# Optimization experiments

Measured on AMD Instinct MI355X. Metric: run time of the kernel, lower is better.

Reference implementation:

```python
import jax, jax.numpy as jnp
import numpy as np

EMB_DIM = 768
HEADS = 12
HEAD_DIM = EMB_DIM // HEADS  # 64


def setup_inputs() -> dict:
    key = jax.random.key(0)
    ks = jax.random.split(key, 9)
    s = 1.0 / np.sqrt(EMB_DIM)
    d = dict(
        x=jax.random.normal(ks[0], (2, 2048, EMB_DIM), dtype=jnp.float32),
        wq_w=jax.random.normal(ks[1], (EMB_DIM, EMB_DIM), dtype=jnp.float32) * s,
        wq_b=jax.random.normal(ks[2], (EMB_DIM,), dtype=jnp.float32) * 0.01,
        wk_w=jax.random.normal(ks[3], (EMB_DIM, EMB_DIM), dtype=jnp.float32) * s,
        wk_b=jax.random.normal(ks[4], (EMB_DIM,), dtype=jnp.float32) * 0.01,
        wv_w=jax.random.normal(ks[5], (EMB_DIM, EMB_DIM), dtype=jnp.float32) * s,
        wv_b=jax.random.normal(ks[6], (EMB_DIM,), dtype=jnp.float32) * 0.01,
        wo_w=jax.random.normal(ks[7], (EMB_DIM, EMB_DIM), dtype=jnp.float32) * s,
        wo_b=jax.random.normal(ks[8], (EMB_DIM,), dtype=jnp.float32) * 0.01,
    )
    return d


def reference(x, wq_w, wq_b, wk_w, wk_b, wv_w, wv_b, wo_w, wo_b):
    b, n, _ = x.shape
    # Linear projections (torch Linear: x @ W^T + b). q scaled by 1/8 == 1/sqrt(head_dim).
    q = (x @ wq_w.T + wq_b) / 8.0
    k = x @ wk_w.T + wk_b
    v = x @ wv_w.T + wv_b
    # [b, h, n, d]
    q = q.reshape(b, n, HEADS, HEAD_DIM).transpose(0, 2, 1, 3)
    k = k.reshape(b, n, HEADS, HEAD_DIM).transpose(0, 2, 1, 3)
    v = v.reshape(b, n, HEADS, HEAD_DIM).transpose(0, 2, 1, 3)
    # Full [b, h, n, n] score matrix with causal mask (strict upper triangle = -inf)
    scores = jnp.einsum('bhqd,bhkd->bhqk', q, k)
    causal = jnp.tril(jnp.ones((n, n), dtype=bool))  # True where allowed
    scores = jnp.where(causal[None, None], scores, -jnp.inf)
    attn = jax.nn.softmax(scores, axis=-1)
    out = jnp.einsum('bhqk,bhkd->bhqd', attn, v)
    out = out.transpose(0, 2, 1, 3).reshape(b, n, EMB_DIM)
    return out @ wo_w.T + wo_b
```

## Files before the change

kernel.cpp:

```cpp
#include <hip/hip_runtime.h>
#include <hip/hip_bf16.h>
#include <math.h>

#define EMB  768
#define NH   12
#define HD   64
#define SEQ  2048
#define BATCH 2
#define NTOK 4096

typedef __attribute__((ext_vector_type(8))) short short8;
typedef __attribute__((ext_vector_type(4))) float float4v;

static __device__ __forceinline__ short f2bf(float f) {
    __hip_bfloat16 h = __float2bfloat16(f);
    return *reinterpret_cast<short*>(&h);
}

static __device__ __forceinline__ void gll16(const void* g, void* l) {
    __builtin_amdgcn_global_load_lds(
        (const __attribute__((address_space(1))) void*)g,
        (__attribute__((address_space(3))) void*)l, 16, 0, 0);
}

__global__ __launch_bounds__(256) void cast_kernel(
    const float* __restrict__ x,  const float* __restrict__ wq,
    const float* __restrict__ wk, const float* __restrict__ wv,
    const float* __restrict__ wo,
    __hip_bfloat16* __restrict__ xb,  __hip_bfloat16* __restrict__ wqb,
    __hip_bfloat16* __restrict__ wkb, __hip_bfloat16* __restrict__ wvb,
    __hip_bfloat16* __restrict__ wob)
{
    const size_t S0 = (size_t)NTOK * EMB;
    const size_t S1 = (size_t)EMB * EMB;
    size_t i = ((size_t)blockIdx.x * 256 + threadIdx.x) * 8;
    const float* src; __hip_bfloat16* dst; size_t off;
    if      (i < S0)            { src = x;  dst = xb;  off = i; }
    else if (i < S0 + S1)       { src = wq; dst = wqb; off = i - S0; }
    else if (i < S0 + 2 * S1)   { src = wk; dst = wkb; off = i - S0 - S1; }
    else if (i < S0 + 3 * S1)   { src = wv; dst = wvb; off = i - S0 - 2 * S1; }
    else                        { src = wo; dst = wob; off = i - S0 - 3 * S1; }
    float4 f0 = *(const float4*)&src[off];
    float4 f1 = *(const float4*)&src[off + 4];
    short8 o;
    o[0] = f2bf(f0.x); o[1] = f2bf(f0.y); o[2] = f2bf(f0.z); o[3] = f2bf(f0.w);
    o[4] = f2bf(f1.x); o[5] = f2bf(f1.y); o[6] = f2bf(f1.z); o[7] = f2bf(f1.w);
    *(short8*)&dst[off] = o;
}

__global__ __launch_bounds__(256) void qkv_mfma_kernel(
    const __hip_bfloat16* __restrict__ xb,
    const __hip_bfloat16* __restrict__ wqb, const float* __restrict__ bq,
    const __hip_bfloat16* __restrict__ wkb, const float* __restrict__ bk,
    const __hip_bfloat16* __restrict__ wvb, const float* __restrict__ bv,
    __hip_bfloat16* __restrict__ q, __hip_bfloat16* __restrict__ k,
    __hip_bfloat16* __restrict__ vT)
{
    __shared__ __align__(16) short SM[12288];
    short* As = SM;
    short* Bs = SM + 4096;
    const int t = threadIdx.x;
    const int w = t >> 6, lane = t & 63;
    const int col = lane & 15, quad = lane >> 4;
    const int wm = w >> 1, wn = w & 1;
    const int m0 = blockIdx.y * 64;
    const int mat = blockIdx.x / 6;
    const int jj0 = (blockIdx.x % 6) * 128;
    const short* X = (const short*)xb;
    const short* W = (const short*)((mat == 0) ? wqb : (mat == 1) ? wkb : wvb);
    const float* bias = (mat == 0) ? bq : (mat == 1) ? bk : bv;

    float4v acc[2][4];
    #pragma unroll
    for (int mi = 0; mi < 2; ++mi)
        #pragma unroll
        for (int ni = 0; ni < 4; ++ni) acc[mi][ni] = (float4v){0.f, 0.f, 0.f, 0.f};

    for (int kb = 0; kb < EMB; kb += 64) {
        #pragma unroll
        for (int c = 0; c < 2; ++c) {
            int I = w * 128 + c * 64 + lane;
            int row = I >> 3;
            int c8 = (I & 7) ^ (row & 7);
            gll16(X + (size_t)(m0 + row) * EMB + kb + c8 * 8,
                  &As[(w * 128 + c * 64) * 8]);
        }
        #pragma unroll
        for (int c = 0; c < 4; ++c) {
            int I = w * 256 + c * 64 + lane;
            int row = I >> 3;
            int c8 = (I & 7) ^ (row & 7);
            gll16(W + (size_t)(jj0 + row) * EMB + kb + c8 * 8,
                  &Bs[(w * 256 + c * 64) * 8]);
        }
        __syncthreads();
        #pragma unroll
        for (int ks = 0; ks < 2; ++ks) {
            short8 a[2], b[4];
            #pragma unroll
            for (int mi = 0; mi < 2; ++mi) {
                int row = wm * 32 + mi * 16 + col;
                a[mi] = *(short8*)&As[row * 64 + (((ks * 4 + quad) ^ (row & 7)) * 8)];
            }
            #pragma unroll
            for (int ni = 0; ni < 4; ++ni) {
                int row = wn * 64 + ni * 16 + col;
                b[ni] = *(short8*)&Bs[row * 64 + (((ks * 4 + quad) ^ (row & 7)) * 8)];
            }
            #pragma unroll
            for (int mi = 0; mi < 2; ++mi)
                #pragma unroll
                for (int ni = 0; ni < 4; ++ni)
                    acc[mi][ni] = __builtin_amdgcn_mfma_f32_16x16x32_bf16(
                        a[mi], b[ni], acc[mi][ni], 0, 0, 0);
        }
        __syncthreads();
    }
    const int bi = m0 >> 11, n0g = m0 & (SEQ - 1);
    if (mat != 2) {
        const float scale = (mat == 0) ? 0.125f * 1.44269504088896f : 1.0f;
        __hip_bfloat16* dstqk = (mat == 0) ? q : k;
        #pragma unroll
        for (int mi = 0; mi < 2; ++mi)
            #pragma unroll
            for (int ni = 0; ni < 4; ++ni) {
                int gj_l = wn * 64 + ni * 16 + col;
                float bsv = bias[jj0 + gj_l];
                #pragma unroll
                for (int r = 0; r < 4; ++r) {
                    int n_l = wm * 32 + mi * 16 + quad * 4 + r;
                    int cswz = (gj_l >> 3) ^ (n_l & 15);
                    SM[(n_l << 7) + (cswz << 3) + (gj_l & 7)] =
                        f2bf((acc[mi][ni][r] + bsv) * scale);
                }
            }
        __syncthreads();
        #pragma unroll
        for (int it = 0; it < 4; ++it) {
            int I = it * 256 + t;
            int n_l = I >> 4, c = I & 15;
            short8 val = *(short8*)&SM[(n_l << 7) + ((c ^ (n_l & 15)) << 3)];
            int gj = jj0 + c * 8;
            int h = gj >> 6, d0 = gj & 63;
            int gm = m0 + n_l;
            int bb = gm >> 11, n = gm & (SEQ - 1);
            *(short8*)&dstqk[(((size_t)bb * NH + h) * SEQ + n) * HD + d0] = val;
        }
    } else {
        #pragma unroll
        for (int mi = 0; mi < 2; ++mi)
            #pragma unroll
            for (int ni = 0; ni < 4; ++ni) {
                int d_l = wn * 64 + ni * 16 + col;
                float bsv = bias[jj0 + d_l];
                #pragma unroll
                for (int r = 0; r < 4; ++r) {
                    int n_l = wm * 32 + mi * 16 + quad * 4 + r;
                    int cn = n_l >> 3;
                    SM[(d_l << 6) + (((cn ^ (d_l & 7))) << 3) + (n_l & 7)] =
                        f2bf(acc[mi][ni][r] + bsv);
                }
            }
        __syncthreads();
        #pragma unroll
        for (int it = 0; it < 4; ++it) {
            int I = it * 256 + t;
            int d_l = I >> 3, cn = I & 7;
            short8 val = *(short8*)&SM[(d_l << 6) + ((cn ^ (d_l & 7)) << 3)];
            int gj = jj0 + d_l;
            int h = gj >> 6, dd = gj & 63;
            *(short8*)&vT[(((size_t)bi * NH + h) * HD + dd) * SEQ + n0g + cn * 8] = val;
        }
    }
}

__global__ __launch_bounds__(256) void attn_mfma_kernel(
    const __hip_bfloat16* __restrict__ qg, const __hip_bfloat16* __restrict__ kg,
    const __hip_bfloat16* __restrict__ vTg, __hip_bfloat16* __restrict__ ao,
    float* __restrict__ Os0, float* __restrict__ Os1,
    float* __restrict__ l0, float* __restrict__ l1)
{
    __shared__ __align__(16) short Ks[2][64 * 64];
    __shared__ __align__(16) short Vt[2][64 * 64];
    __shared__ __align__(16) short Ps[4][32][72];
    const int t = threadIdx.x;
    const int w = t >> 6, lane = t & 63;
    const int col = lane & 15, quad = lane >> 4;
    const int id = blockIdx.x;
    const int bh = id % 24;
    const int x = id / 24;
    int b, c;
    if (x < 8) { b = 8 + x; c = 0; }
    else {
        int i = x - 8, j = i >> 1;
        if ((i & 1) == 0) { b = 7 - j;  c = 0; }
        else              { b = 15 - j; c = 1; }
    }
    const int kt0 = c * 16;
    const int ktend = (kt0 + 16 < 2 * b + 2) ? kt0 + 16 : 2 * b + 2;
    const int niter = ktend - kt0;
    const bool single = (b <= 7);
    const int q0 = b * 128;
    const size_t base = (size_t)bh * SEQ * HD;
    const short* kp = (const short*)kg + base;
    const short* vp = (const short*)vTg + base;
    const short* qp = (const short*)qg + base;

    short8 qa[2][2];
    #pragma unroll
    for (int mi = 0; mi < 2; ++mi) {
        int qrow = q0 + (2 * w + mi) * 16 + col;
        #pragma unroll
        for (int ks = 0; ks < 2; ++ks)
            qa[mi][ks] = *(const short8*)&qp[(size_t)qrow * HD + ks * 32 + quad * 8];
    }
    float4v accO[2][4];
    float lacc[2][4];
    #pragma unroll
    for (int mi = 0; mi < 2; ++mi) {
        #pragma unroll
        for (int di = 0; di < 4; ++di) accO[mi][di] = (float4v){0.f, 0.f, 0.f, 0.f};
        #pragma unroll
        for (int r = 0; r < 4; ++r) lacc[mi][r] = 0.f;
    }

    {
        const int k0 = kt0 * 64;
        #pragma unroll
        for (int cc = 0; cc < 2; ++cc) {
            int I = w * 128 + cc * 64 + lane;
            int row = I >> 3;
            int c8 = (I & 7) ^ (row & 7);
            gll16(kp + (size_t)(k0 + row) * HD + c8 * 8, &Ks[0][(w * 128 + cc * 64) * 8]);
            gll16(vp + (size_t)row * SEQ + k0 + c8 * 8, &Vt[0][(w * 128 + cc * 64) * 8]);
        }
    }

    for (int lk = 0; lk < niter; ++lk) {
        const int kt = kt0 + lk;
        const int cur = lk & 1;
        const int k0 = kt * 64;
        __syncthreads();
        if (lk + 1 < niter) {
            const int kn = k0 + 64;
            #pragma unroll
            for (int cc = 0; cc < 2; ++cc) {
                int I = w * 128 + cc * 64 + lane;
                int row = I >> 3;
                int c8 = (I & 7) ^ (row & 7);
                gll16(kp + (size_t)(kn + row) * HD + c8 * 8,
                      &Ks[cur ^ 1][(w * 128 + cc * 64) * 8]);
                gll16(vp + (size_t)row * SEQ + kn + c8 * 8,
                      &Vt[cur ^ 1][(w * 128 + cc * 64) * 8]);
            }
        }
        const short* Kc = &Ks[cur][0];
        const short* Vc = &Vt[cur][0];

        float4v s[2][4];
        #pragma unroll
        for (int mi = 0; mi < 2; ++mi)
            #pragma unroll
            for (int ni = 0; ni < 4; ++ni) s[mi][ni] = (float4v){0.f, 0.f, 0.f, 0.f};
        #pragma unroll
        for (int ks = 0; ks < 2; ++ks)
            #pragma unroll
            for (int ni = 0; ni < 4; ++ni) {
                int row = ni * 16 + col;
                short8 kf = *(short8*)&Kc[row * 64 + (((ks * 4 + quad) ^ (row & 7)) * 8)];
                #pragma unroll
                for (int mi = 0; mi < 2; ++mi)
                    s[mi][ni] = __builtin_amdgcn_mfma_f32_16x16x32_bf16(
                        qa[mi][ks], kf, s[mi][ni], 0, 0, 0);
            }

        if (k0 >= q0) {
            #pragma unroll
            for (int mi = 0; mi < 2; ++mi)
                #pragma unroll
                for (int ni = 0; ni < 4; ++ni) {
                    int gcol = k0 + ni * 16 + col;
                    #pragma unroll
                    for (int r = 0; r < 4; ++r) {
                        int grow = q0 + (2 * w + mi) * 16 + quad * 4 + r;
                        s[mi][ni][r] = (gcol > grow) ? 0.f : exp2f(s[mi][ni][r]);
                    }
                }
        } else {
            #pragma unroll
            for (int mi = 0; mi < 2; ++mi)
                #pragma unroll
                for (int ni = 0; ni < 4; ++ni)
                    #pragma unroll
                    for (int r = 0; r < 4; ++r)
                        s[mi][ni][r] = exp2f(s[mi][ni][r]);
        }
        #pragma unroll
        for (int mi = 0; mi < 2; ++mi)
            #pragma unroll
            for (int r = 0; r < 4; ++r)
                lacc[mi][r] += (s[mi][0][r] + s[mi][1][r]) + (s[mi][2][r] + s[mi][3][r]);

        #pragma unroll
        for (int mi = 0; mi < 2; ++mi)
            #pragma unroll
            for (int ni = 0; ni < 4; ++ni)
                #pragma unroll
                for (int r = 0; r < 4; ++r)
                    Ps[w][mi * 16 + quad * 4 + r][ni * 16 + col] = f2bf(s[mi][ni][r]);
        short8 pa[2][2];
        #pragma unroll
        for (int mi = 0; mi < 2; ++mi)
            #pragma unroll
            for (int ks = 0; ks < 2; ++ks)
                pa[mi][ks] = *(short8*)&Ps[w][mi * 16 + col][ks * 32 + quad * 8];

        #pragma unroll
        for (int ks = 0; ks < 2; ++ks)
            #pragma unroll
            for (int di = 0; di < 4; ++di) {
                int row = di * 16 + col;
                short8 vf = *(short8*)&Vc[row * 64 + (((ks * 4 + quad) ^ (row & 7)) * 8)];
                #pragma unroll
                for (int mi = 0; mi < 2; ++mi)
                    accO[mi][di] = __builtin_amdgcn_mfma_f32_16x16x32_bf16(
                        pa[mi][ks], vf, accO[mi][di], 0, 0, 0);
            }
    }

    #pragma unroll
    for (int msk = 1; msk < 16; msk <<= 1)
        #pragma unroll
        for (int mi = 0; mi < 2; ++mi)
            #pragma unroll
            for (int r = 0; r < 4; ++r)
                lacc[mi][r] += __shfl_xor(lacc[mi][r], msk);

    const int bi = bh / NH, h = bh % NH;
    if (single) {
        #pragma unroll
        for (int mi = 0; mi < 2; ++mi)
            #pragma unroll
            for (int r = 0; r < 4; ++r) {
                float inv = 1.0f / lacc[mi][r];
                int n = q0 + (2 * w + mi) * 16 + quad * 4 + r;
                #pragma unroll
                for (int di = 0; di < 4; ++di)
                    ao[((size_t)bi * SEQ + n) * EMB + h * HD + di * 16 + col] =
                        __float2bfloat16(accO[mi][di][r] * inv);
            }
    } else {
        float* Os = c ? Os1 : Os0;
        float* ls = c ? l1 : l0;
        #pragma unroll
        for (int mi = 0; mi < 2; ++mi)
            #pragma unroll
            for (int r = 0; r < 4; ++r) {
                int n = q0 + (2 * w + mi) * 16 + quad * 4 + r;
                int nn = n - 1024;
                size_t rowb = ((size_t)bi * 1024 + nn) * EMB + h * HD;
                #pragma unroll
                for (int di = 0; di < 4; ++di)
                    Os[rowb + di * 16 + col] = accO[mi][di][r];
                if (col == 0)
                    ls[((size_t)bi * 1024 + nn) * NH + h] = lacc[mi][r];
            }
    }
}

__global__ __launch_bounds__(256) void combine_kernel(
    const float* __restrict__ Os0, const float* __restrict__ Os1,
    const float* __restrict__ l0, const float* __restrict__ l1,
    __hip_bfloat16* __restrict__ ao)
{
    size_t e8 = ((size_t)blockIdx.x * 256 + threadIdx.x) * 8;
    int u = e8 / EMB;
    int within = e8 % EMB;
    int h = within >> 6;
    int bi = u >> 10, nn = u & 1023;
    float inv = 1.0f / (l0[(size_t)u * NH + h] + l1[(size_t)u * NH + h]);
    float4 a0 = *(const float4*)&Os0[e8];
    float4 a1 = *(const float4*)&Os0[e8 + 4];
    float4 b0 = *(const float4*)&Os1[e8];
    float4 b1 = *(const float4*)&Os1[e8 + 4];
    short8 o;
    o[0] = f2bf((a0.x + b0.x) * inv); o[1] = f2bf((a0.y + b0.y) * inv);
    o[2] = f2bf((a0.z + b0.z) * inv); o[3] = f2bf((a0.w + b0.w) * inv);
    o[4] = f2bf((a1.x + b1.x) * inv); o[5] = f2bf((a1.y + b1.y) * inv);
    o[6] = f2bf((a1.z + b1.z) * inv); o[7] = f2bf((a1.w + b1.w) * inv);
    *(short8*)&ao[((size_t)bi * SEQ + 1024 + nn) * EMB + within] = o;
}

__global__ __launch_bounds__(256) void out_proj_mfma_kernel(
    const __hip_bfloat16* __restrict__ a, const __hip_bfloat16* __restrict__ wob,
    const float* __restrict__ bias, float* __restrict__ out)
{
    __shared__ __align__(16) short As[64 * 64];
    __shared__ __align__(16) short Bs[64 * 64];
    const int t = threadIdx.x;
    const int w = t >> 6, lane = t & 63;
    const int col = lane & 15, quad = lane >> 4;
    const int wm = w >> 1, wn = w & 1;
    const int m0 = blockIdx.y * 64;
    const int n0 = blockIdx.x * 64;
    const short* A = (const short*)a;
    const short* W = (const short*)wob;

    float4v acc[2][2];
    #pragma unroll
    for (int mi = 0; mi < 2; ++mi)
        #pragma unroll
        for (int ni = 0; ni < 2; ++ni) acc[mi][ni] = (float4v){0.f, 0.f, 0.f, 0.f};

    for (int kb = 0; kb < EMB; kb += 64) {
        #pragma unroll
        for (int c = 0; c < 2; ++c) {
            int I = w * 128 + c * 64 + lane;
            int row = I >> 3;
            int c8 = (I & 7) ^ (row & 7);
            gll16(A + (size_t)(m0 + row) * EMB + kb + c8 * 8,
                  &As[(w * 128 + c * 64) * 8]);
            gll16(W + (size_t)(n0 + row) * EMB + kb + c8 * 8,
                  &Bs[(w * 128 + c * 64) * 8]);
        }
        __syncthreads();
        #pragma unroll
        for (int ks = 0; ks < 2; ++ks) {
            short8 av[2], bv[2];
            #pragma unroll
            for (int mi = 0; mi < 2; ++mi) {
                int row = wm * 32 + mi * 16 + col;
                av[mi] = *(short8*)&As[row * 64 + (((ks * 4 + quad) ^ (row & 7)) * 8)];
            }
            #pragma unroll
            for (int ni = 0; ni < 2; ++ni) {
                int row = wn * 32 + ni * 16 + col;
                bv[ni] = *(short8*)&Bs[row * 64 + (((ks * 4 + quad) ^ (row & 7)) * 8)];
            }
            #pragma unroll
            for (int mi = 0; mi < 2; ++mi)
                #pragma unroll
                for (int ni = 0; ni < 2; ++ni)
                    acc[mi][ni] = __builtin_amdgcn_mfma_f32_16x16x32_bf16(
                        av[mi], bv[ni], acc[mi][ni], 0, 0, 0);
        }
        __syncthreads();
    }
    #pragma unroll
    for (int mi = 0; mi < 2; ++mi)
        #pragma unroll
        for (int ni = 0; ni < 2; ++ni) {
            int gj = n0 + wn * 32 + ni * 16 + col;
            float bsv = bias[gj];
            #pragma unroll
            for (int r = 0; r < 4; ++r) {
                int gm = m0 + wm * 32 + mi * 16 + quad * 4 + r;
                out[(size_t)gm * EMB + gj] = acc[mi][ni][r] + bsv;
            }
        }
}

extern "C" void kernel_launch(void* const* d_in, const int* in_sizes, int n_in,
                              void* d_out, int out_size, void* d_ws, size_t ws_size,
                              hipStream_t stream) {
    const float* x  = (const float*)d_in[0];
    const float* wq = (const float*)d_in[1];
    const float* bq = (const float*)d_in[2];
    const float* wk = (const float*)d_in[3];
    const float* bk = (const float*)d_in[4];
    const float* wv = (const float*)d_in[5];
    const float* bv = (const float*)d_in[6];
    const float* wo = (const float*)d_in[7];
    const float* bo = (const float*)d_in[8];
    float* out = (float*)d_out;

    const size_t TOK = (size_t)NTOK * EMB;
    const size_t WSZ = (size_t)EMB * EMB;
    __hip_bfloat16* xb  = (__hip_bfloat16*)d_ws;
    __hip_bfloat16* wqb = xb  + TOK;
    __hip_bfloat16* wkb = wqb + WSZ;
    __hip_bfloat16* wvb = wkb + WSZ;
    __hip_bfloat16* wob = wvb + WSZ;
    __hip_bfloat16* qb  = wob + WSZ;
    __hip_bfloat16* kb  = qb  + TOK;
    __hip_bfloat16* vTb = kb  + TOK;
    __hip_bfloat16* aob = vTb + TOK;
    float* Os0 = (float*)d_ws;
    float* Os1 = (float*)(aob + TOK);
    float* l0  = Os1 + (size_t)2 * 1024 * EMB;
    float* l1  = l0  + (size_t)2 * 1024 * NH;

    cast_kernel<<<2688, 256, 0, stream>>>(x, wq, wk, wv, wo, xb, wqb, wkb, wvb, wob);
    qkv_mfma_kernel<<<dim3(18, 64), 256, 0, stream>>>(xb, wqb, bq, wkb, bk, wvb, bv,
                                                      qb, kb, vTb);
    attn_mfma_kernel<<<576, 256, 0, stream>>>(qb, kb, vTb, aob, Os0, Os1, l0, l1);
    combine_kernel<<<768, 256, 0, stream>>>(Os0, Os1, l0, l1, aob);
    out_proj_mfma_kernel<<<dim3(12, 64), 256, 0, stream>>>(aob, wob, bo, out);
}
```

Before: 164.7 us.

## Use 256-row query blocks with up to four key-chunk splits in attention

Attention blocks now cover 256 query rows (64 per wave) instead of 128, and the key range is split into chunks of 8 tiles, giving up to four partial results per block that the combine kernel sums. This doubles Q reuse per loaded K/V tile and interleaves the QK and PV matmuls per 32-key half with a smaller P scratch buffer. Waves skip tiles lying fully above their diagonal. In exchange it writes and reads more fp32 partials in workspace, uses more registers per thread, and launches fewer attention blocks.

Measured after the change: 186.9 us. +13.5%, slower.

```diff
diff --git a/kernel.cpp b/kernel.cpp
--- a/kernel.cpp
+++ b/kernel.cpp
@@ -22,6 +22,9 @@
         (const __attribute__((address_space(1))) void*)g,
         (__attribute__((address_space(3))) void*)l, 16, 0, 0);
 }
+
+__device__ const int BS8[16] = {1,2,3,3,4,4,5,5,5,6,6,6,7,7,7,7};
+__device__ const int CS8[16] = {0,0,0,1,0,1,0,1,2,0,1,2,0,1,2,3};
 
 __global__ __launch_bounds__(256) void cast_kernel(
     const float* __restrict__ x,  const float* __restrict__ wq,
@@ -177,12 +180,11 @@
 __global__ __launch_bounds__(256) void attn_mfma_kernel(
     const __hip_bfloat16* __restrict__ qg, const __hip_bfloat16* __restrict__ kg,
     const __hip_bfloat16* __restrict__ vTg, __hip_bfloat16* __restrict__ ao,
-    float* __restrict__ Os0, float* __restrict__ Os1,
-    float* __restrict__ l0, float* __restrict__ l1)
+    float* __restrict__ Osp, float* __restrict__ lsp)
 {
-    __shared__ __align__(16) short Ks[2][64 * 64];
-    __shared__ __align__(16) short Vt[2][64 * 64];
-    __shared__ __align__(16) short Ps[4][32][72];
+    __shared__ __align__(16) short Ks[2][4096];
+    __shared__ __align__(16) short Vt[2][4096];
+    __shared__ __align__(16) short Ps[4][64 * 40];
     const int t = threadIdx.x;
     const int w = t >> 6, lane = t & 63;
     const int col = lane & 15, quad = lane >> 4;
@@ -190,34 +192,31 @@
     const int bh = id % 24;
     const int x = id / 24;
     int b, c;
-    if (x < 8) { b = 8 + x; c = 0; }
-    else {
-        int i = x - 8, j = i >> 1;
-        if ((i & 1) == 0) { b = 7 - j;  c = 0; }
-        else              { b = 15 - j; c = 1; }
-    }
-    const int kt0 = c * 16;
-    const int ktend = (kt0 + 16 < 2 * b + 2) ? kt0 + 16 : 2 * b + 2;
-    const int niter = ktend - kt0;
-    const bool single = (b <= 7);
-    const int q0 = b * 128;
+    if (x < 16) { b = BS8[x]; c = CS8[x]; }
+    else        { int i = x - 16; b = 2 * i; c = i; }
+    const int kt0 = c * 8;
+    const int tottiles = 4 * b + 4;
+    const int niter = (tottiles - kt0 < 8) ? (tottiles - kt0) : 8;
+    const bool single = (b <= 1);
+    const int q0 = b * 256;
     const size_t base = (size_t)bh * SEQ * HD;
     const short* kp = (const short*)kg + base;
     const short* vp = (const short*)vTg + base;
     const short* qp = (const short*)qg + base;
-
-    short8 qa[2][2];
-    #pragma unroll
-    for (int mi = 0; mi < 2; ++mi) {
-        int qrow = q0 + (2 * w + mi) * 16 + col;
+    const int rw = q0 + w * 64;
+
+    short8 qa[4][2];
+    #pragma unroll
+    for (int mi = 0; mi < 4; ++mi) {
+        int qrow = rw + mi * 16 + col;
         #pragma unroll
         for (int ks = 0; ks < 2; ++ks)
             qa[mi][ks] = *(const short8*)&qp[(size_t)qrow * HD + ks * 32 + quad * 8];
     }
-    float4v accO[2][4];
-    float lacc[2][4];
-    #pragma unroll
-    for (int mi = 0; mi < 2; ++mi) {
+    float4v accO[4][4];
+    float lacc[4][4];
+    #pragma unroll
+    for (int mi = 0; mi < 4; ++mi) {
         #pragma unroll
         for (int di = 0; di < 4; ++di) accO[mi][di] = (float4v){0.f, 0.f, 0.f, 0.f};
         #pragma unroll
@@ -254,84 +253,70 @@
                       &Vt[cur ^ 1][(w * 128 + cc * 64) * 8]);
             }
         }
+        if (k0 > rw) continue;
+        const bool diag = (k0 == rw);
         const short* Kc = &Ks[cur][0];
         const short* Vc = &Vt[cur][0];
-
-        float4v s[2][4];
-        #pragma unroll
-        for (int mi = 0; mi < 2; ++mi)
-            #pragma unroll
-            for (int ni = 0; ni < 4; ++ni) s[mi][ni] = (float4v){0.f, 0.f, 0.f, 0.f};
-        #pragma unroll
-        for (int ks = 0; ks < 2; ++ks)
-            #pragma unroll
-            for (int ni = 0; ni < 4; ++ni) {
-                int row = ni * 16 + col;
-                short8 kf = *(short8*)&Kc[row * 64 + (((ks * 4 + quad) ^ (row & 7)) * 8)];
-                #pragma unroll
-                for (int mi = 0; mi < 2; ++mi)
-                    s[mi][ni] = __builtin_amdgcn_mfma_f32_16x16x32_bf16(
-                        qa[mi][ks], kf, s[mi][ni], 0, 0, 0);
-            }
-
-        if (k0 >= q0) {
-            #pragma unroll
-            for (int mi = 0; mi < 2; ++mi)
-                #pragma unroll
-                for (int ni = 0; ni < 4; ++ni) {
-                    int gcol = k0 + ni * 16 + col;
+        short* Pw = &Ps[w][0];
+
+        #pragma unroll
+        for (int ni = 0; ni < 4; ++ni) {
+            float4v s[4];
+            #pragma unroll
+            for (int mi = 0; mi < 4; ++mi) s[mi] = (float4v){0.f, 0.f, 0.f, 0.f};
+            int krow = ni * 16 + col;
+            #pragma unroll
+            for (int ks = 0; ks < 2; ++ks) {
+                short8 kf = *(short8*)&Kc[krow * 64 + (((ks * 4 + quad) ^ (krow & 7)) * 8)];
+                #pragma unroll
+                for (int mi = 0; mi < 4; ++mi)
+                    s[mi] = __builtin_amdgcn_mfma_f32_16x16x32_bf16(
+                        qa[mi][ks], kf, s[mi], 0, 0, 0);
+            }
+            if (diag) {
+                int gcol = k0 + ni * 16 + col;
+                #pragma unroll
+                for (int mi = 0; mi < 4; ++mi)
                     #pragma unroll
                     for (int r = 0; r < 4; ++r) {
-                        int grow = q0 + (2 * w + mi) * 16 + quad * 4 + r;
-                        s[mi][ni][r] = (gcol > grow) ? 0.f : exp2f(s[mi][ni][r]);
+                        int grow = rw + mi * 16 + quad * 4 + r;
+                        float p = (gcol > grow) ? 0.f : exp2f(s[mi][r]);
+                        lacc[mi][r] += p;
+                        Pw[(mi * 16 + quad * 4 + r) * 40 + (ni & 1) * 16 + col] = f2bf(p);
                     }
+            } else {
+                #pragma unroll
+                for (int mi = 0; mi < 4; ++mi)
+                    #pragma unroll
+                    for (int r = 0; r < 4; ++r) {
+                        float p = exp2f(s[mi][r]);
+                        lacc[mi][r] += p;
+                        Pw[(mi * 16 + quad * 4 + r) * 40 + (ni & 1) * 16 + col] = f2bf(p);
+                    }
+            }
+            if (ni & 1) {
+                const int half = ni >> 1;
+                short8 pa[4];
+                #pragma unroll
+                for (int mi = 0; mi < 4; ++mi)
+                    pa[mi] = *(short8*)&Pw[(mi * 16 + col) * 40 + quad * 8];
+                #pragma unroll
+                for (int di = 0; di < 4; ++di) {
+                    int vrow = di * 16 + col;
+                    short8 vf = *(short8*)&Vc[vrow * 64 + (((half * 4 + quad) ^ (vrow & 7)) * 8)];
+                    #pragma unroll
+                    for (int mi = 0; mi < 4; ++mi)
+                        accO[mi][di] = __builtin_amdgcn_mfma_f32_16x16x32_bf16(
+                            pa[mi], vf, accO[mi][di], 0, 0, 0);
                 }
-        } else {
-            #pragma unroll
-            for (int mi = 0; mi < 2; ++mi)
-                #pragma unroll
-                for (int ni = 0; ni < 4; ++ni)
-                    #pragma unroll
-                    for (int r = 0; r < 4; ++r)
-                        s[mi][ni][r] = exp2f(s[mi][ni][r]);
-        }
-        #pragma unroll
-        for (int mi = 0; mi < 2; ++mi)
-            #pragma unroll
-            for (int r = 0; r < 4; ++r)
-                lacc[mi][r] += (s[mi][0][r] + s[mi][1][r]) + (s[mi][2][r] + s[mi][3][r]);
-
-        #pragma unroll
-        for (int mi = 0; mi < 2; ++mi)
-            #pragma unroll
-            for (int ni = 0; ni < 4; ++ni)
-                #pragma unroll
-                for (int r = 0; r < 4; ++r)
-                    Ps[w][mi * 16 + quad * 4 + r][ni * 16 + col] = f2bf(s[mi][ni][r]);
-        short8 pa[2][2];
-        #pragma unroll
-        for (int mi = 0; mi < 2; ++mi)
-            #pragma unroll
-            for (int ks = 0; ks < 2; ++ks)
-                pa[mi][ks] = *(short8*)&Ps[w][mi * 16 + col][ks * 32 + quad * 8];
-
-        #pragma unroll
-        for (int ks = 0; ks < 2; ++ks)
-            #pragma unroll
-            for (int di = 0; di < 4; ++di) {
-                int row = di * 16 + col;
-                short8 vf = *(short8*)&Vc[row * 64 + (((ks * 4 + quad) ^ (row & 7)) * 8)];
-                #pragma unroll
-                for (int mi = 0; mi < 2; ++mi)
-                    accO[mi][di] = __builtin_amdgcn_mfma_f32_16x16x32_bf16(
-                        pa[mi][ks], vf, accO[mi][di], 0, 0, 0);
-            }
+            }
+        }
     }
 
     #pragma unroll
     for (int msk = 1; msk < 16; msk <<= 1)
         #pragma unroll
-        for (int mi = 0; mi < 2; ++mi)
+        for (int mi = 0; mi < 4; ++mi)
             #pragma unroll
             for (int r = 0; r < 4; ++r)
                 lacc[mi][r] += __shfl_xor(lacc[mi][r], msk);
@@ -339,56 +324,67 @@
     const int bi = bh / NH, h = bh % NH;
     if (single) {
         #pragma unroll
-        for (int mi = 0; mi < 2; ++mi)
+        for (int mi = 0; mi < 4; ++mi)
             #pragma unroll
             for (int r = 0; r < 4; ++r) {
                 float inv = 1.0f / lacc[mi][r];
-                int n = q0 + (2 * w + mi) * 16 + quad * 4 + r;
+                int n = rw + mi * 16 + quad * 4 + r;
                 #pragma unroll
                 for (int di = 0; di < 4; ++di)
                     ao[((size_t)bi * SEQ + n) * EMB + h * HD + di * 16 + col] =
                         __float2bfloat16(accO[mi][di][r] * inv);
             }
     } else {
-        float* Os = c ? Os1 : Os0;
-        float* ls = c ? l1 : l0;
-        #pragma unroll
-        for (int mi = 0; mi < 2; ++mi)
+        float* Os = Osp + (size_t)c * 2 * 1536 * EMB;
+        float* ls = lsp + (size_t)c * 2 * 1536 * NH;
+        #pragma unroll
+        for (int mi = 0; mi < 4; ++mi)
             #pragma unroll
             for (int r = 0; r < 4; ++r) {
-                int n = q0 + (2 * w + mi) * 16 + quad * 4 + r;
-                int nn = n - 1024;
-                size_t rowb = ((size_t)bi * 1024 + nn) * EMB + h * HD;
+                int n = rw + mi * 16 + quad * 4 + r;
+                int nn = n - 512;
+                size_t rowb = ((size_t)bi * 1536 + nn) * EMB + h * HD;
                 #pragma unroll
                 for (int di = 0; di < 4; ++di)
                     Os[rowb + di * 16 + col] = accO[mi][di][r];
                 if (col == 0)
-                    ls[((size_t)bi * 1024 + nn) * NH + h] = lacc[mi][r];
+                    ls[((size_t)bi * 1536 + nn) * NH + h] = lacc[mi][r];
             }
     }
 }
 
 __global__ __launch_bounds__(256) void combine_kernel(
-    const float* __restrict__ Os0, const float* __restrict__ Os1,
-    const float* __restrict__ l0, const float* __restrict__ l1,
+    const float* __restrict__ Osp, const float* __restrict__ lsp,
     __hip_bfloat16* __restrict__ ao)
 {
+    const size_t SLOT = (size_t)2 * 1536 * EMB;
+    const size_t LSLOT = (size_t)2 * 1536 * NH;
     size_t e8 = ((size_t)blockIdx.x * 256 + threadIdx.x) * 8;
     int u = e8 / EMB;
     int within = e8 % EMB;
     int h = within >> 6;
-    int bi = u >> 10, nn = u & 1023;
-    float inv = 1.0f / (l0[(size_t)u * NH + h] + l1[(size_t)u * NH + h]);
-    float4 a0 = *(const float4*)&Os0[e8];
-    float4 a1 = *(const float4*)&Os0[e8 + 4];
-    float4 b0 = *(const float4*)&Os1[e8];
-    float4 b1 = *(const float4*)&Os1[e8 + 4];
+    int bi = u / 1536, nn = u % 1536;
+    int n = 512 + nn;
+    int qb = n >> 8;
+    int nc = (qb >> 1) + 1;
+    float4 a0 = *(const float4*)&Osp[e8];
+    float4 a1 = *(const float4*)&Osp[e8 + 4];
+    float lsum = lsp[(size_t)u * NH + h];
+    for (int cc = 1; cc < nc; ++cc) {
+        const float* O = Osp + (size_t)cc * SLOT;
+        float4 b0 = *(const float4*)&O[e8];
+        float4 b1 = *(const float4*)&O[e8 + 4];
+        a0.x += b0.x; a0.y += b0.y; a0.z += b0.z; a0.w += b0.w;
+        a1.x += b1.x; a1.y += b1.y; a1.z += b1.z; a1.w += b1.w;
+        lsum += lsp[(size_t)cc * LSLOT + (size_t)u * NH + h];
+    }
+    float inv = 1.0f / lsum;
     short8 o;
-    o[0] = f2bf((a0.x + b0.x) * inv); o[1] = f2bf((a0.y + b0.y) * inv);
-    o[2] = f2bf((a0.z + b0.z) * inv); o[3] = f2bf((a0.w + b0.w) * inv);
-    o[4] = f2bf((a1.x + b1.x) * inv); o[5] = f2bf((a1.y + b1.y) * inv);
-    o[6] = f2bf((a1.z + b1.z) * inv); o[7] = f2bf((a1.w + b1.w) * inv);
-    *(short8*)&ao[((size_t)bi * SEQ + 1024 + nn) * EMB + within] = o;
+    o[0] = f2bf(a0.x * inv); o[1] = f2bf(a0.y * inv);
+    o[2] = f2bf(a0.z * inv); o[3] = f2bf(a0.w * inv);
+    o[4] = f2bf(a1.x * inv); o[5] = f2bf(a1.y * inv);
+    o[6] = f2bf(a1.z * inv); o[7] = f2bf(a1.w * inv);
+    *(short8*)&ao[((size_t)bi * SEQ + n) * EMB + within] = o;
 }
 
 __global__ __launch_bounds__(256) void out_proj_mfma_kernel(
@@ -485,15 +481,13 @@
     __hip_bfloat16* kb  = qb  + TOK;
     __hip_bfloat16* vTb = kb  + TOK;
     __hip_bfloat16* aob = vTb + TOK;
-    float* Os0 = (float*)d_ws;
-    float* Os1 = (float*)(aob + TOK);
-    float* l0  = Os1 + (size_t)2 * 1024 * EMB;
-    float* l1  = l0  + (size_t)2 * 1024 * NH;
+    float* Osp = (float*)(aob + TOK);
+    float* lsp = Osp + (size_t)4 * 2 * 1536 * EMB;
 
     cast_kernel<<<2688, 256, 0, stream>>>(x, wq, wk, wv, wo, xb, wqb, wkb, wvb, wob);
     qkv_mfma_kernel<<<dim3(18, 64), 256, 0, stream>>>(xb, wqb, bq, wkb, bk, wvb, bv,
                                                       qb, kb, vTb);
-    attn_mfma_kernel<<<576, 256, 0, stream>>>(qb, kb, vTb, aob, Os0, Os1, l0, l1);
-    combine_kernel<<<768, 256, 0, stream>>>(Os0, Os1, l0, l1, aob);
+    attn_mfma_kernel<<<480, 256, 0, stream>>>(qb, kb, vTb, aob, Osp, lsp);
+    combine_kernel<<<1152, 256, 0, stream>>>(Osp, lsp, aob);
     out_proj_mfma_kernel<<<dim3(12, 64), 256, 0, stream>>>(aob, wob, bo, out);
 }
```

## Split causal attention KV range into four chunks with table-driven scheduling

Applied to the files above, without the earlier changes.

Changes the split-K attention from two KV halves of 16 tiles to up to four chunks of 8 tiles each. Query blocks 4 and above are split, and a lookup table orders the work items so the longest ones are scheduled first. The goal is to even out per-block work and raise the block count (576 to 960) for better CU utilization on the causal triangle. In exchange, more fp32 partial results must be written and then reduced by a larger combine kernel, which adds memory traffic and workspace.

After: 160.6 us. -2.5%, faster.

```diff
diff --git a/kernel.cpp b/kernel.cpp
--- a/kernel.cpp
+++ b/kernel.cpp
@@ -22,6 +22,23 @@
         (const __attribute__((address_space(1))) void*)g,
         (__attribute__((address_space(3))) void*)l, 16, 0, 0);
 }
+
+__device__ const unsigned char UB[40] = {
+    3,4,5,6,7,8,9,10,11,12,13,14,15,
+    7,8,9,10,11,12,13,14,15,
+    11,12,13,14,15,
+    15,
+    2,6,10,14,
+    1,5,9,13,
+    0,4,8,12};
+__device__ const unsigned char UC[40] = {
+    0,0,0,0,0,0,0,0,0,0,0,0,0,
+    1,1,1,1,1,1,1,1,1,
+    2,2,2,2,2,
+    3,
+    0,1,2,3,
+    0,1,2,3,
+    0,1,2,3};
 
 __global__ __launch_bounds__(256) void cast_kernel(
     const float* __restrict__ x,  const float* __restrict__ wq,
@@ -177,8 +194,7 @@
 __global__ __launch_bounds__(256) void attn_mfma_kernel(
     const __hip_bfloat16* __restrict__ qg, const __hip_bfloat16* __restrict__ kg,
     const __hip_bfloat16* __restrict__ vTg, __hip_bfloat16* __restrict__ ao,
-    float* __restrict__ Os0, float* __restrict__ Os1,
-    float* __restrict__ l0, float* __restrict__ l1)
+    float* __restrict__ Osp, float* __restrict__ lsp)
 {
     __shared__ __align__(16) short Ks[2][64 * 64];
     __shared__ __align__(16) short Vt[2][64 * 64];
@@ -189,17 +205,11 @@
     const int id = blockIdx.x;
     const int bh = id % 24;
     const int x = id / 24;
-    int b, c;
-    if (x < 8) { b = 8 + x; c = 0; }
-    else {
-        int i = x - 8, j = i >> 1;
-        if ((i & 1) == 0) { b = 7 - j;  c = 0; }
-        else              { b = 15 - j; c = 1; }
-    }
-    const int kt0 = c * 16;
-    const int ktend = (kt0 + 16 < 2 * b + 2) ? kt0 + 16 : 2 * b + 2;
-    const int niter = ktend - kt0;
-    const bool single = (b <= 7);
+    const int b = UB[x], c = UC[x];
+    const int kt0 = c * 8;
+    const int tottiles = 2 * b + 2;
+    const int niter = (tottiles - kt0 < 8) ? (tottiles - kt0) : 8;
+    const bool single = (b <= 3);
     const int q0 = b * 128;
     const size_t base = (size_t)bh * SEQ * HD;
     const short* kp = (const short*)kg + base;
@@ -350,45 +360,56 @@
                         __float2bfloat16(accO[mi][di][r] * inv);
             }
     } else {
-        float* Os = c ? Os1 : Os0;
-        float* ls = c ? l1 : l0;
+        float* Os = Osp + (size_t)c * 2 * 1536 * EMB;
+        float* ls = lsp + (size_t)c * 2 * 1536 * NH;
         #pragma unroll
         for (int mi = 0; mi < 2; ++mi)
             #pragma unroll
             for (int r = 0; r < 4; ++r) {
                 int n = q0 + (2 * w + mi) * 16 + quad * 4 + r;
-                int nn = n - 1024;
-                size_t rowb = ((size_t)bi * 1024 + nn) * EMB + h * HD;
+                int nn = n - 512;
+                size_t rowb = ((size_t)bi * 1536 + nn) * EMB + h * HD;
                 #pragma unroll
                 for (int di = 0; di < 4; ++di)
                     Os[rowb + di * 16 + col] = accO[mi][di][r];
                 if (col == 0)
-                    ls[((size_t)bi * 1024 + nn) * NH + h] = lacc[mi][r];
+                    ls[((size_t)bi * 1536 + nn) * NH + h] = lacc[mi][r];
             }
     }
 }
 
 __global__ __launch_bounds__(256) void combine_kernel(
-    const float* __restrict__ Os0, const float* __restrict__ Os1,
-    const float* __restrict__ l0, const float* __restrict__ l1,
+    const float* __restrict__ Osp, const float* __restrict__ lsp,
     __hip_bfloat16* __restrict__ ao)
 {
+    const size_t SLOT = (size_t)2 * 1536 * EMB;
+    const size_t LSLOT = (size_t)2 * 1536 * NH;
     size_t e8 = ((size_t)blockIdx.x * 256 + threadIdx.x) * 8;
     int u = e8 / EMB;
     int within = e8 % EMB;
     int h = within >> 6;
-    int bi = u >> 10, nn = u & 1023;
-    float inv = 1.0f / (l0[(size_t)u * NH + h] + l1[(size_t)u * NH + h]);
-    float4 a0 = *(const float4*)&Os0[e8];
-    float4 a1 = *(const float4*)&Os0[e8 + 4];
-    float4 b0 = *(const float4*)&Os1[e8];
-    float4 b1 = *(const float4*)&Os1[e8 + 4];
+    int bi = u / 1536, nn = u % 1536;
+    int n = 512 + nn;
+    int qb = n >> 7;
+    int nc = (2 * qb + 9) >> 3;
+    float4 a0 = *(const float4*)&Osp[e8];
+    float4 a1 = *(const float4*)&Osp[e8 + 4];
+    float lsum = lsp[(size_t)u * NH + h];
+    for (int cc = 1; cc < nc; ++cc) {
+        const float* O = Osp + (size_t)cc * SLOT;
+        float4 b0 = *(const float4*)&O[e8];
+        float4 b1 = *(const float4*)&O[e8 + 4];
+        a0.x += b0.x; a0.y += b0.y; a0.z += b0.z; a0.w += b0.w;
+        a1.x += b1.x; a1.y += b1.y; a1.z += b1.z; a1.w += b1.w;
+        lsum += lsp[(size_t)cc * LSLOT + (size_t)u * NH + h];
+    }
+    float inv = 1.0f / lsum;
     short8 o;
-    o[0] = f2bf((a0.x + b0.x) * inv); o[1] = f2bf((a0.y + b0.y) * inv);
-    o[2] = f2bf((a0.z + b0.z) * inv); o[3] = f2bf((a0.w + b0.w) * inv);
-    o[4] = f2bf((a1.x + b1.x) * inv); o[5] = f2bf((a1.y + b1.y) * inv);
-    o[6] = f2bf((a1.z + b1.z) * inv); o[7] = f2bf((a1.w + b1.w) * inv);
-    *(short8*)&ao[((size_t)bi * SEQ + 1024 + nn) * EMB + within] = o;
+    o[0] = f2bf(a0.x * inv); o[1] = f2bf(a0.y * inv);
+    o[2] = f2bf(a0.z * inv); o[3] = f2bf(a0.w * inv);
+    o[4] = f2bf(a1.x * inv); o[5] = f2bf(a1.y * inv);
+    o[6] = f2bf(a1.z * inv); o[7] = f2bf(a1.w * inv);
+    *(short8*)&ao[((size_t)bi * SEQ + n) * EMB + within] = o;
 }
 
 __global__ __launch_bounds__(256) void out_proj_mfma_kernel(
@@ -485,15 +506,13 @@
     __hip_bfloat16* kb  = qb  + TOK;
     __hip_bfloat16* vTb = kb  + TOK;
     __hip_bfloat16* aob = vTb + TOK;
-    float* Os0 = (float*)d_ws;
-    float* Os1 = (float*)(aob + TOK);
-    float* l0  = Os1 + (size_t)2 * 1024 * EMB;
-    float* l1  = l0  + (size_t)2 * 1024 * NH;
+    float* Osp = (float*)(aob + TOK);
+    float* lsp = Osp + (size_t)4 * 2 * 1536 * EMB;
 
     cast_kernel<<<2688, 256, 0, stream>>>(x, wq, wk, wv, wo, xb, wqb, wkb, wvb, wob);
     qkv_mfma_kernel<<<dim3(18, 64), 256, 0, stream>>>(xb, wqb, bq, wkb, bk, wvb, bv,
                                                       qb, kb, vTb);
-    attn_mfma_kernel<<<576, 256, 0, stream>>>(qb, kb, vTb, aob, Os0, Os1, l0, l1);
-    combine_kernel<<<768, 256, 0, stream>>>(Os0, Os1, l0, l1, aob);
+    attn_mfma_kernel<<<960, 256, 0, stream>>>(qb, kb, vTb, aob, Osp, lsp);
+    combine_kernel<<<1152, 256, 0, stream>>>(Osp, lsp, aob);
     out_proj_mfma_kernel<<<dim3(12, 64), 256, 0, stream>>>(aob, wob, bo, out);
 }
```
